# Kernel optimization log

Hardware: AMD Instinct MI355X
Metric: run time of the kernel (lower is better)

## Reference

```python
import jax, jax.numpy as jnp
import numpy as np

N = 50000
E = 800000
NFEAT, NHID, NCLASS = 256, 128, 32


def setup_inputs() -> dict:
    key = jax.random.key(0)
    ks = jax.random.split(key, 8)
    x = jax.random.normal(ks[0], (N, NFEAT), dtype=jnp.float32)
    edge_src = jax.random.randint(ks[1], (E,), 0, N, dtype=jnp.int32)
    edge_dst = jax.random.randint(ks[2], (E,), 0, N, dtype=jnp.int32)
    edge_weight = jax.random.uniform(ks[3], (E,), dtype=jnp.float32)
    # Linear layer params (torch Linear: y = x @ W.T + b); store as [in, out]
    s1 = 1.0 / np.sqrt(NFEAT)
    s2 = 1.0 / np.sqrt(NHID)
    W1 = jax.random.uniform(ks[4], (NFEAT, NHID), jnp.float32, -s1, s1)
    b1 = jax.random.uniform(ks[5], (NHID,), jnp.float32, -s1, s1)
    W2 = jax.random.uniform(ks[6], (NHID, NCLASS), jnp.float32, -s2, s2)
    b2 = jax.random.uniform(ks[7], (NCLASS,), jnp.float32, -s2, s2)
    return {"x": x, "edge_src": edge_src, "edge_dst": edge_dst,
            "edge_weight": edge_weight, "W1": W1, "b1": b1, "W2": W2, "b2": b2}


def spmm(edge_src, edge_dst, edge_weight, h):
    # out[dst] += w * h[src]  -- sparse adjacency @ dense features
    msgs = edge_weight[:, None] * h[edge_src]          # [E, F]
    return jax.ops.segment_sum(msgs, edge_dst, num_segments=N)


def reference(x, edge_src, edge_dst, edge_weight, W1, b1, W2, b2):
    # GCN layer 1: Linear -> SpMM -> ReLU (dropout inactive in eval mode)
    h = x @ W1 + b1                                    # [N, NHID]
    h = spmm(edge_src, edge_dst, edge_weight, h)
    h = jax.nn.relu(h)
    # GCN layer 2: Linear -> SpMM
    h = h @ W2 + b2                                    # [N, NCLASS]
    out = spmm(edge_src, edge_dst, edge_weight, h)
    return out
```

## Files before the change

### kernel.cpp

```cpp
#include <hip/hip_runtime.h>

#define NFEAT 256
#define NHID 128
#define NCLASS 32

typedef __attribute__((ext_vector_type(8))) short short8;
typedef __attribute__((ext_vector_type(4))) float f32x4;
typedef __attribute__((ext_vector_type(4))) int int4v;

static __device__ __forceinline__ unsigned short f2bf(float f) {
    unsigned u = __float_as_uint(f);
    unsigned r = (u + 0x7fffu + ((u >> 16) & 1u)) >> 16;
    return (unsigned short)r;
}
static __device__ __forceinline__ float bf_lo(unsigned d) {
    return __uint_as_float(d << 16);
}
static __device__ __forceinline__ float bf_hi(unsigned d) {
    return __uint_as_float(d & 0xffff0000u);
}

__global__ __launch_bounds__(256) void prep_kernel(
    const float* __restrict__ W1, unsigned short* __restrict__ W1t,
    const int* __restrict__ dst, int* __restrict__ bkt_partial,
    int E, int CE, int shift)
{
    const int tid = threadIdx.x;
    if (blockIdx.x < 128) {
        int o = blockIdx.x * 256 + tid;
        int c = o >> 8, k = o & 255;
        W1t[o] = f2bf(W1[(size_t)k * NHID + c]);
    } else {
        __shared__ int h[256];
        const int kb = blockIdx.x - 128;
        const int start = kb * CE;
        const int end = min(start + CE, E);
        h[tid] = 0;
        __syncthreads();
        for (int e4 = start + tid * 4; e4 < end; e4 += 1024) {
            if (e4 + 3 < end) {
                int4 d4 = *(const int4*)&dst[e4];
                atomicAdd(&h[d4.x >> shift], 1);
                atomicAdd(&h[d4.y >> shift], 1);
                atomicAdd(&h[d4.z >> shift], 1);
                atomicAdd(&h[d4.w >> shift], 1);
            } else {
                for (int e = e4; e < end; ++e)
                    atomicAdd(&h[dst[e] >> shift], 1);
            }
        }
        __syncthreads();
        bkt_partial[kb * 256 + tid] = h[tid];
    }
}

__global__ __launch_bounds__(256) void scan_kernel(
    const int* __restrict__ bkt_partial, int* __restrict__ chunk_pre,
    int* __restrict__ bkt_base, int E)
{
    __shared__ int s[256];
    const int t = threadIdx.x;
    int run = 0;
    for (int kb = 0; kb < 256; ++kb) {
        chunk_pre[kb * 256 + t] = run;
        run += bkt_partial[kb * 256 + t];
    }
    s[t] = run;
    __syncthreads();
    for (int off = 1; off < 256; off <<= 1) {
        int tv = (t >= off) ? s[t - off] : 0;
        __syncthreads();
        s[t] += tv;
        __syncthreads();
    }
    bkt_base[t] = s[t] - run;
    if (t == 255) bkt_base[256] = s[255];
}

__global__ __launch_bounds__(256) void bucket_scatter_kernel(
    const int* __restrict__ src, const int* __restrict__ dst,
    const float* __restrict__ w, const int* __restrict__ bkt_base,
    const int* __restrict__ chunk_pre, uint2* __restrict__ bkt_edges,
    int E, int CE, int shift)
{
    __shared__ int cur[256];
    const int tid = threadIdx.x;
    const int kb = blockIdx.x;
    cur[tid] = bkt_base[tid] + chunk_pre[kb * 256 + tid];
    __syncthreads();
    const int start = kb * CE;
    const int end = min(start + CE, E);
    const unsigned lmask = (1u << shift) - 1u;
    for (int e4 = start + tid * 4; e4 < end; e4 += 1024) {
        if (e4 + 3 < end) {
            int4 d4 = *(const int4*)&dst[e4];
            int4 s4 = *(const int4*)&src[e4];
            float4 w4 = *(const float4*)&w[e4];
            int dd[4] = {d4.x, d4.y, d4.z, d4.w};
            int ss[4] = {s4.x, s4.y, s4.z, s4.w};
            float ww[4] = {w4.x, w4.y, w4.z, w4.w};
#pragma unroll
            for (int j = 0; j < 4; ++j) {
                int b = dd[j] >> shift;
                int pos = atomicAdd(&cur[b], 1);
                uint2 rec;
                rec.x = (unsigned)ss[j] | (((unsigned)dd[j] & lmask) << 24);
                rec.y = __float_as_uint(ww[j]);
                bkt_edges[pos] = rec;
            }
        } else {
            for (int e = e4; e < end; ++e) {
                int d = dst[e];
                int b = d >> shift;
                int pos = atomicAdd(&cur[b], 1);
                uint2 rec;
                rec.x = (unsigned)src[e] | (((unsigned)d & lmask) << 24);
                rec.y = __float_as_uint(w[e]);
                bkt_edges[pos] = rec;
            }
        }
    }
}

__global__ __launch_bounds__(1024) void fine_scatter_kernel(
    const int* __restrict__ bkt_base, const uint2* __restrict__ bkt_edges,
    int* __restrict__ row_ptr, uint2* __restrict__ csr_e,
    int shift, int N, int E)
{
    __shared__ int h[256];
    __shared__ int cur[256];
    const int b = blockIdx.x;
    const int t = threadIdx.x;
    const int lo = bkt_base[b], hi = bkt_base[b + 1];
    const int dbase = b << shift;

    if (t < 256) h[t] = 0;
    __syncthreads();
    for (int i = lo + t; i < hi; i += 1024)
        atomicAdd(&h[bkt_edges[i].x >> 24], 1);
    __syncthreads();
    int v = (t < 256) ? h[t] : 0;
    for (int off = 1; off < 256; off <<= 1) {
        int tv = (t >= off && t < 256) ? h[t - off] : 0;
        __syncthreads();
        if (t < 256) h[t] += tv;
        __syncthreads();
    }
    if (t < 256) {
        int excl = h[t] - v;
        int r = dbase + t;
        if (r < N) row_ptr[r] = lo + excl;
        cur[t] = lo + excl;
    }
    if (b == 0 && t == 0) row_ptr[N] = E;
    __syncthreads();
    for (int i = lo + t; i < hi; i += 1024) {
        uint2 rec = bkt_edges[i];
        int dl = rec.x >> 24;
        int pos = atomicAdd(&cur[dl], 1);
        uint2 o;
        o.x = rec.x & 0xFFFFFFu;
        o.y = rec.y;
        csr_e[pos] = o;
    }
}

__global__ __launch_bounds__(256) void gemm1_mfma_kernel(
    const float* __restrict__ x, const unsigned short* __restrict__ W1t,
    const float* __restrict__ b1, unsigned short* __restrict__ h1b, int N)
{
    __shared__ unsigned short wt[128 * 64];
    __shared__ unsigned short xs[64 * 64];

    const int tid = threadIdx.x;
    const int lane = tid & 63;
    const int wv = tid >> 6;
    const int row0 = blockIdx.x * 64;
    const int l15 = lane & 15;
    const int l47 = lane >> 4;
    const int r7 = lane & 7;

    auto stage_wt = [&](int t) {
#pragma unroll
        for (int j = 0; j < 4; ++j) {
            int si = tid + j * 256;
            int c = si >> 3, s = si & 7;
            int sp = s ^ (c & 7);
            const int4v* wsrc = (const int4v*)(W1t + (size_t)c * 256 + t * 64);
            int4v v = wsrc[s];
            *(int4v*)&wt[c * 64 + sp * 8] = v;
        }
    };
    auto stage_x = [&](int t) {
#pragma unroll
        for (int j = 0; j < 2; ++j) {
            int si = tid + j * 256;
            int r = si >> 3, s = si & 7;
            int row = row0 + r;
            float4 v0 = make_float4(0.f, 0.f, 0.f, 0.f), v1 = v0;
            if (row < N) {
                const float4* xp = (const float4*)&x[(size_t)row * NFEAT + t * 64 + s * 8];
                v0 = xp[0]; v1 = xp[1];
            }
            int w0 = f2bf(v0.x) | ((unsigned)f2bf(v0.y) << 16);
            int w1 = f2bf(v0.z) | ((unsigned)f2bf(v0.w) << 16);
            int w2 = f2bf(v1.x) | ((unsigned)f2bf(v1.y) << 16);
            int w3 = f2bf(v1.z) | ((unsigned)f2bf(v1.w) << 16);
            int sp = s ^ (r & 7);
            int4v pv; pv[0] = w0; pv[1] = w1; pv[2] = w2; pv[3] = w3;
            *(int4v*)&xs[r * 64 + sp * 8] = pv;
        }
    };

    f32x4 acc[8];
#pragma unroll
    for (int cf = 0; cf < 8; ++cf)
#pragma unroll
        for (int r = 0; r < 4; ++r) acc[cf][r] = 0.f;

    const int arow = wv * 16 + l15;
#pragma unroll
    for (int t = 0; t < 4; ++t) {
        stage_wt(t);
        stage_x(t);
        __syncthreads();
        short8 af[2];
#pragma unroll
        for (int kf = 0; kf < 2; ++kf) {
            int slot = (kf * 4 + l47) ^ r7;
            af[kf] = *(const short8*)&xs[arow * 64 + slot * 8];
        }
#pragma unroll
        for (int cf = 0; cf < 8; ++cf) {
            const int brow = cf * 16 + l15;
#pragma unroll
            for (int kf = 0; kf < 2; ++kf) {
                int slot = (kf * 4 + l47) ^ r7;
                short8 bfr = *(const short8*)&wt[brow * 64 + slot * 8];
                acc[cf] = __builtin_amdgcn_mfma_f32_16x16x32_bf16(af[kf], bfr, acc[cf], 0, 0, 0);
            }
        }
        __syncthreads();
    }

#pragma unroll
    for (int cf = 0; cf < 8; ++cf) {
        float bias = b1[cf * 16 + l15];
#pragma unroll
        for (int r = 0; r < 4; ++r) {
            int row = row0 + wv * 16 + l47 * 4 + r;
            if (row < N)
                h1b[(size_t)row * NHID + cf * 16 + l15] = f2bf(acc[cf][r] + bias);
        }
    }
}

__global__ __launch_bounds__(512) void spmm1_gemm2_kernel(
    const int* __restrict__ row_ptr, const uint2* __restrict__ csr_e,
    const unsigned short* __restrict__ h1b, const float* __restrict__ W2,
    const float* __restrict__ b2, unsigned* __restrict__ h2b, int N)
{
    __shared__ float w2s[NHID * NCLASS];
    __shared__ float hrow[8][NHID];
    const int tid = threadIdx.x;
#pragma unroll
    for (int j = 0; j < 8; ++j) {
        int idx = tid + j * 512;
        w2s[idx] = W2[idx];
    }
    __syncthreads();

    const int lane = tid & 63;
    const int wv = tid >> 6;
    const int row = __builtin_amdgcn_readfirstlane(blockIdx.x * 8 + wv);
    if (row >= N) return;

    const int e0 = row_ptr[row], e1 = row_ptr[row + 1];
    const size_t loff = (size_t)(lane * 2);
    float a0 = 0.f, a1 = 0.f;
    int e = e0;
    for (; e + 8 <= e1; e += 8) {
        uint2 r[8];
#pragma unroll
        for (int j = 0; j < 8; ++j) r[j] = csr_e[e + j];
        unsigned d[8];
#pragma unroll
        for (int j = 0; j < 8; ++j)
            d[j] = *(const unsigned*)(h1b + (size_t)r[j].x * NHID + loff);
#pragma unroll
        for (int j = 0; j < 8; ++j) {
            float w = __uint_as_float(r[j].y);
            a0 += w * bf_lo(d[j]); a1 += w * bf_hi(d[j]);
        }
    }
    if (e + 4 <= e1) {
        uint2 r[4];
#pragma unroll
        for (int j = 0; j < 4; ++j) r[j] = csr_e[e + j];
        unsigned d[4];
#pragma unroll
        for (int j = 0; j < 4; ++j)
            d[j] = *(const unsigned*)(h1b + (size_t)r[j].x * NHID + loff);
#pragma unroll
        for (int j = 0; j < 4; ++j) {
            float w = __uint_as_float(r[j].y);
            a0 += w * bf_lo(d[j]); a1 += w * bf_hi(d[j]);
        }
        e += 4;
    }
    if (e + 2 <= e1) {
        uint2 r0 = csr_e[e], r1 = csr_e[e + 1];
        unsigned d0 = *(const unsigned*)(h1b + (size_t)r0.x * NHID + loff);
        unsigned d1 = *(const unsigned*)(h1b + (size_t)r1.x * NHID + loff);
        float w0 = __uint_as_float(r0.y), w1 = __uint_as_float(r1.y);
        a0 += w0 * bf_lo(d0); a1 += w0 * bf_hi(d0);
        a0 += w1 * bf_lo(d1); a1 += w1 * bf_hi(d1);
        e += 2;
    }
    if (e < e1) {
        uint2 r = csr_e[e];
        float w = __uint_as_float(r.y);
        unsigned d = *(const unsigned*)(h1b + (size_t)r.x * NHID + loff);
        a0 += w * bf_lo(d); a1 += w * bf_hi(d);
    }
    *(float2*)&hrow[wv][lane * 2] = make_float2(fmaxf(a0, 0.f), fmaxf(a1, 0.f));

    const int c = lane & 31;
    const int kh = lane >> 5;
    const float* hw = &hrow[wv][kh * 64];
    const float* wp = &w2s[(size_t)kh * 64 * NCLASS + c];
    float acc = 0.f;
#pragma unroll
    for (int k = 0; k < 64; ++k)
        acc += hw[k] * wp[k * NCLASS];
    acc += __shfl(acc, lane ^ 32);
    float accb = acc + b2[c];
    float nb = __shfl(accb, lane ^ 1);
    if (kh == 0 && (lane & 1) == 0) {
        unsigned u = (unsigned)f2bf(accb) | ((unsigned)f2bf(nb) << 16);
        h2b[(size_t)row * 16 + (lane >> 1)] = u;
    }
}

__global__ __launch_bounds__(256) void spmm2_kernel(
    const int* __restrict__ row_ptr, const uint2* __restrict__ csr_e,
    const unsigned* __restrict__ h2b, float* __restrict__ out, int N)
{
    const int li = threadIdx.x & 15;
    const int g = threadIdx.x >> 4;
    const int row = blockIdx.x * 16 + g;
    if (row >= N) return;
    const int e0 = row_ptr[row], e1 = row_ptr[row + 1];
    float a0 = 0.f, a1 = 0.f;
    int e = e0;
    for (; e + 16 <= e1; e += 16) {
        uint2 r[16];
#pragma unroll
        for (int j = 0; j < 16; ++j) r[j] = csr_e[e + j];
        unsigned d[16];
#pragma unroll
        for (int j = 0; j < 16; ++j) d[j] = h2b[(size_t)r[j].x * 16 + li];
#pragma unroll
        for (int j = 0; j < 16; ++j) {
            float w = __uint_as_float(r[j].y);
            a0 += w * bf_lo(d[j]); a1 += w * bf_hi(d[j]);
        }
    }
    for (; e + 8 <= e1; e += 8) {
        uint2 r[8];
#pragma unroll
        for (int j = 0; j < 8; ++j) r[j] = csr_e[e + j];
        unsigned d[8];
#pragma unroll
        for (int j = 0; j < 8; ++j) d[j] = h2b[(size_t)r[j].x * 16 + li];
#pragma unroll
        for (int j = 0; j < 8; ++j) {
            float w = __uint_as_float(r[j].y);
            a0 += w * bf_lo(d[j]); a1 += w * bf_hi(d[j]);
        }
    }
    for (; e + 2 <= e1; e += 2) {
        uint2 r0 = csr_e[e], r1 = csr_e[e + 1];
        unsigned d0 = h2b[(size_t)r0.x * 16 + li];
        unsigned d1 = h2b[(size_t)r1.x * 16 + li];
        float w0 = __uint_as_float(r0.y), w1 = __uint_as_float(r1.y);
        a0 += w0 * bf_lo(d0); a1 += w0 * bf_hi(d0);
        a0 += w1 * bf_lo(d1); a1 += w1 * bf_hi(d1);
    }
    if (e < e1) {
        uint2 r = csr_e[e];
        float w = __uint_as_float(r.y);
        unsigned d = h2b[(size_t)r.x * 16 + li];
        a0 += w * bf_lo(d); a1 += w * bf_hi(d);
    }
    *(float2*)&out[(size_t)row * NCLASS + li * 2] = make_float2(a0, a1);
}


extern "C" void kernel_launch(void* const* d_in, const int* in_sizes, int n_in,
                              void* d_out, int out_size, void* d_ws, size_t ws_size,
                              hipStream_t stream) {
    const float* x    = (const float*)d_in[0];
    const int*   esrc = (const int*)d_in[1];
    const int*   edst = (const int*)d_in[2];
    const float* ew   = (const float*)d_in[3];
    const float* W1   = (const float*)d_in[4];
    const float* b1   = (const float*)d_in[5];
    const float* W2   = (const float*)d_in[6];
    const float* b2   = (const float*)d_in[7];
    float* out = (float*)d_out;

    const int N = in_sizes[0] / NFEAT;
    const int E = in_sizes[1];

    int shift = 0;
    while (((N - 1) >> shift) >= 256) ++shift;
    const int NBKT = ((N - 1) >> shift) + 1;
    const int CE = (((E + 255) / 256) + 3) & ~3;

    char* base = (char*)d_ws;
    size_t off = 0;
    auto take = [&](size_t bytes) -> void* {
        void* p = base + off;
        off += (bytes + 255) & ~(size_t)255;
        return p;
    };
    unsigned short* h1b = (unsigned short*)take((size_t)N * NHID * sizeof(unsigned short));
    unsigned* h2b  = (unsigned*)take((size_t)N * 16 * sizeof(unsigned));
    int*   row_ptr = (int*)take((size_t)(N + 1) * sizeof(int));
    int*   bkt_partial = (int*)take(256 * 256 * sizeof(int));
    int*   chunk_pre   = (int*)take(256 * 256 * sizeof(int));
    int*   bkt_base    = (int*)take(257 * sizeof(int));
    uint2* bkt_edges   = (uint2*)take((size_t)E * sizeof(uint2));
    uint2* csr_e       = (uint2*)take((size_t)E * sizeof(uint2));
    unsigned short* W1t = (unsigned short*)take((size_t)NFEAT * NHID * sizeof(unsigned short));
    (void)ws_size; (void)n_in; (void)out_size;

    prep_kernel<<<384, 256, 0, stream>>>(W1, W1t, edst, bkt_partial, E, CE, shift);
    scan_kernel<<<1, 256, 0, stream>>>(bkt_partial, chunk_pre, bkt_base, E);
    bucket_scatter_kernel<<<256, 256, 0, stream>>>(esrc, edst, ew, bkt_base, chunk_pre,
                                                   bkt_edges, E, CE, shift);
    fine_scatter_kernel<<<NBKT, 1024, 0, stream>>>(bkt_base, bkt_edges, row_ptr, csr_e,
                                                   shift, N, E);
    gemm1_mfma_kernel<<<(N + 63) / 64, 256, 0, stream>>>(x, W1t, b1, h1b, N);
    spmm1_gemm2_kernel<<<(N + 7) / 8, 512, 0, stream>>>(row_ptr, csr_e, h1b, W2, b2, h2b, N);
    spmm2_kernel<<<(N + 15) / 16, 256, 0, stream>>>(row_ptr, csr_e, h2b, out, N);
}
```

Before: 102.7 us.

## Merge bucket scatter and GEMM1 into one launch with block-role dispatch

Combines the coarse edge bucket-scatter kernel and the first MFMA GEMM into a single launch. The first 256 blocks do the scatter and the rest compute GEMM tiles, with shared memory unioned between the two roles. The aim is to run the latency-bound atomic scatter alongside the compute-heavy GEMM and save one kernel launch. The cost is that the scatter blocks now reserve the GEMM's larger shared-memory footprint, which may lower their occupancy.

Result: slower. 111.1 us (+8.1%).

```diff
diff --git a/kernel.cpp b/kernel.cpp
--- a/kernel.cpp
+++ b/kernel.cpp
@@ -77,105 +77,62 @@
     if (t == 255) bkt_base[256] = s[255];
 }
 
-__global__ __launch_bounds__(256) void bucket_scatter_kernel(
+__global__ __launch_bounds__(256) void gemm1_scatter_kernel(
+    const float* __restrict__ x, const unsigned short* __restrict__ W1t,
+    const float* __restrict__ b1, unsigned short* __restrict__ h1b, int N,
     const int* __restrict__ src, const int* __restrict__ dst,
     const float* __restrict__ w, const int* __restrict__ bkt_base,
     const int* __restrict__ chunk_pre, uint2* __restrict__ bkt_edges,
     int E, int CE, int shift)
 {
-    __shared__ int cur[256];
+    __shared__ union SM {
+        struct { unsigned short wt[128 * 64]; unsigned short xs[64 * 64]; } g;
+        int cur[256];
+    } sm;
     const int tid = threadIdx.x;
-    const int kb = blockIdx.x;
-    cur[tid] = bkt_base[tid] + chunk_pre[kb * 256 + tid];
-    __syncthreads();
-    const int start = kb * CE;
-    const int end = min(start + CE, E);
-    const unsigned lmask = (1u << shift) - 1u;
-    for (int e4 = start + tid * 4; e4 < end; e4 += 1024) {
-        if (e4 + 3 < end) {
-            int4 d4 = *(const int4*)&dst[e4];
-            int4 s4 = *(const int4*)&src[e4];
-            float4 w4 = *(const float4*)&w[e4];
-            int dd[4] = {d4.x, d4.y, d4.z, d4.w};
-            int ss[4] = {s4.x, s4.y, s4.z, s4.w};
-            float ww[4] = {w4.x, w4.y, w4.z, w4.w};
-#pragma unroll
-            for (int j = 0; j < 4; ++j) {
-                int b = dd[j] >> shift;
-                int pos = atomicAdd(&cur[b], 1);
-                uint2 rec;
-                rec.x = (unsigned)ss[j] | (((unsigned)dd[j] & lmask) << 24);
-                rec.y = __float_as_uint(ww[j]);
-                bkt_edges[pos] = rec;
+
+    if (blockIdx.x < 256) {
+        const int kb = blockIdx.x;
+        sm.cur[tid] = bkt_base[tid] + chunk_pre[kb * 256 + tid];
+        __syncthreads();
+        const int start = kb * CE;
+        const int end = min(start + CE, E);
+        const unsigned lmask = (1u << shift) - 1u;
+        for (int e4 = start + tid * 4; e4 < end; e4 += 1024) {
+            if (e4 + 3 < end) {
+                int4 d4 = *(const int4*)&dst[e4];
+                int4 s4 = *(const int4*)&src[e4];
+                float4 w4 = *(const float4*)&w[e4];
+                int dd[4] = {d4.x, d4.y, d4.z, d4.w};
+                int ss[4] = {s4.x, s4.y, s4.z, s4.w};
+                float ww[4] = {w4.x, w4.y, w4.z, w4.w};
+#pragma unroll
+                for (int j = 0; j < 4; ++j) {
+                    int b = dd[j] >> shift;
+                    int pos = atomicAdd(&sm.cur[b], 1);
+                    uint2 rec;
+                    rec.x = (unsigned)ss[j] | (((unsigned)dd[j] & lmask) << 24);
+                    rec.y = __float_as_uint(ww[j]);
+                    bkt_edges[pos] = rec;
+                }
+            } else {
+                for (int e = e4; e < end; ++e) {
+                    int d = dst[e];
+                    int b = d >> shift;
+                    int pos = atomicAdd(&sm.cur[b], 1);
+                    uint2 rec;
+                    rec.x = (unsigned)src[e] | (((unsigned)d & lmask) << 24);
+                    rec.y = __float_as_uint(w[e]);
+                    bkt_edges[pos] = rec;
+                }
             }
-        } else {
-            for (int e = e4; e < end; ++e) {
-                int d = dst[e];
-                int b = d >> shift;
-                int pos = atomicAdd(&cur[b], 1);
-                uint2 rec;
-                rec.x = (unsigned)src[e] | (((unsigned)d & lmask) << 24);
-                rec.y = __float_as_uint(w[e]);
-                bkt_edges[pos] = rec;
-            }
-        }
-    }
-}
-
-__global__ __launch_bounds__(1024) void fine_scatter_kernel(
-    const int* __restrict__ bkt_base, const uint2* __restrict__ bkt_edges,
-    int* __restrict__ row_ptr, uint2* __restrict__ csr_e,
-    int shift, int N, int E)
-{
-    __shared__ int h[256];
-    __shared__ int cur[256];
-    const int b = blockIdx.x;
-    const int t = threadIdx.x;
-    const int lo = bkt_base[b], hi = bkt_base[b + 1];
-    const int dbase = b << shift;
-
-    if (t < 256) h[t] = 0;
-    __syncthreads();
-    for (int i = lo + t; i < hi; i += 1024)
-        atomicAdd(&h[bkt_edges[i].x >> 24], 1);
-    __syncthreads();
-    int v = (t < 256) ? h[t] : 0;
-    for (int off = 1; off < 256; off <<= 1) {
-        int tv = (t >= off && t < 256) ? h[t - off] : 0;
-        __syncthreads();
-        if (t < 256) h[t] += tv;
-        __syncthreads();
-    }
-    if (t < 256) {
-        int excl = h[t] - v;
-        int r = dbase + t;
-        if (r < N) row_ptr[r] = lo + excl;
-        cur[t] = lo + excl;
-    }
-    if (b == 0 && t == 0) row_ptr[N] = E;
-    __syncthreads();
-    for (int i = lo + t; i < hi; i += 1024) {
-        uint2 rec = bkt_edges[i];
-        int dl = rec.x >> 24;
-        int pos = atomicAdd(&cur[dl], 1);
-        uint2 o;
-        o.x = rec.x & 0xFFFFFFu;
-        o.y = rec.y;
-        csr_e[pos] = o;
-    }
-}
-
-__global__ __launch_bounds__(256) void gemm1_mfma_kernel(
-    const float* __restrict__ x, const unsigned short* __restrict__ W1t,
-    const float* __restrict__ b1, unsigned short* __restrict__ h1b, int N)
-{
-    __shared__ unsigned short wt[128 * 64];
-    __shared__ unsigned short xs[64 * 64];
-
-    const int tid = threadIdx.x;
+        }
+        return;
+    }
+
     const int lane = tid & 63;
     const int wv = tid >> 6;
-    const int row0 = blockIdx.x * 64;
+    const int row0 = (blockIdx.x - 256) * 64;
     const int l15 = lane & 15;
     const int l47 = lane >> 4;
     const int r7 = lane & 7;
@@ -188,7 +145,7 @@
             int sp = s ^ (c & 7);
             const int4v* wsrc = (const int4v*)(W1t + (size_t)c * 256 + t * 64);
             int4v v = wsrc[s];
-            *(int4v*)&wt[c * 64 + sp * 8] = v;
+            *(int4v*)&sm.g.wt[c * 64 + sp * 8] = v;
         }
     };
     auto stage_x = [&](int t) {
@@ -208,7 +165,7 @@
             int w3 = f2bf(v1.z) | ((unsigned)f2bf(v1.w) << 16);
             int sp = s ^ (r & 7);
             int4v pv; pv[0] = w0; pv[1] = w1; pv[2] = w2; pv[3] = w3;
-            *(int4v*)&xs[r * 64 + sp * 8] = pv;
+            *(int4v*)&sm.g.xs[r * 64 + sp * 8] = pv;
         }
     };
 
@@ -228,7 +185,7 @@
 #pragma unroll
         for (int kf = 0; kf < 2; ++kf) {
             int slot = (kf * 4 + l47) ^ r7;
-            af[kf] = *(const short8*)&xs[arow * 64 + slot * 8];
+            af[kf] = *(const short8*)&sm.g.xs[arow * 64 + slot * 8];
         }
 #pragma unroll
         for (int cf = 0; cf < 8; ++cf) {
@@ -236,7 +193,7 @@
 #pragma unroll
             for (int kf = 0; kf < 2; ++kf) {
                 int slot = (kf * 4 + l47) ^ r7;
-                short8 bfr = *(const short8*)&wt[brow * 64 + slot * 8];
+                short8 bfr = *(const short8*)&sm.g.wt[brow * 64 + slot * 8];
                 acc[cf] = __builtin_amdgcn_mfma_f32_16x16x32_bf16(af[kf], bfr, acc[cf], 0, 0, 0);
             }
         }
@@ -252,6 +209,49 @@
             if (row < N)
                 h1b[(size_t)row * NHID + cf * 16 + l15] = f2bf(acc[cf][r] + bias);
         }
+    }
+}
+
+__global__ __launch_bounds__(1024) void fine_scatter_kernel(
+    const int* __restrict__ bkt_base, const uint2* __restrict__ bkt_edges,
+    int* __restrict__ row_ptr, uint2* __restrict__ csr_e,
+    int shift, int N, int E)
+{
+    __shared__ int h[256];
+    __shared__ int cur[256];
+    const int b = blockIdx.x;
+    const int t = threadIdx.x;
+    const int lo = bkt_base[b], hi = bkt_base[b + 1];
+    const int dbase = b << shift;
+
+    if (t < 256) h[t] = 0;
+    __syncthreads();
+    for (int i = lo + t; i < hi; i += 1024)
+        atomicAdd(&h[bkt_edges[i].x >> 24], 1);
+    __syncthreads();
+    int v = (t < 256) ? h[t] : 0;
+    for (int off = 1; off < 256; off <<= 1) {
+        int tv = (t >= off && t < 256) ? h[t - off] : 0;
+        __syncthreads();
+        if (t < 256) h[t] += tv;
+        __syncthreads();
+    }
+    if (t < 256) {
+        int excl = h[t] - v;
+        int r = dbase + t;
+        if (r < N) row_ptr[r] = lo + excl;
+        cur[t] = lo + excl;
+    }
+    if (b == 0 && t == 0) row_ptr[N] = E;
+    __syncthreads();
+    for (int i = lo + t; i < hi; i += 1024) {
+        uint2 rec = bkt_edges[i];
+        int dl = rec.x >> 24;
+        int pos = atomicAdd(&cur[dl], 1);
+        uint2 o;
+        o.x = rec.x & 0xFFFFFFu;
+        o.y = rec.y;
+        csr_e[pos] = o;
     }
 }
 
@@ -417,6 +417,7 @@
     while (((N - 1) >> shift) >= 256) ++shift;
     const int NBKT = ((N - 1) >> shift) + 1;
     const int CE = (((E + 255) / 256) + 3) & ~3;
+    const int ntiles = (N + 63) / 64;
 
     char* base = (char*)d_ws;
     size_t off = 0;
@@ -438,11 +439,10 @@
 
     prep_kernel<<<384, 256, 0, stream>>>(W1, W1t, edst, bkt_partial, E, CE, shift);
     scan_kernel<<<1, 256, 0, stream>>>(bkt_partial, chunk_pre, bkt_base, E);
-    bucket_scatter_kernel<<<256, 256, 0, stream>>>(esrc, edst, ew, bkt_base, chunk_pre,
-                                                   bkt_edges, E, CE, shift);
+    gemm1_scatter_kernel<<<256 + ntiles, 256, 0, stream>>>(
+        x, W1t, b1, h1b, N, esrc, edst, ew, bkt_base, chunk_pre, bkt_edges, E, CE, shift);
     fine_scatter_kernel<<<NBKT, 1024, 0, stream>>>(bkt_base, bkt_edges, row_ptr, csr_e,
                                                    shift, N, E);
-    gemm1_mfma_kernel<<<(N + 63) / 64, 256, 0, stream>>>(x, W1t, b1, h1b, N);
     spmm1_gemm2_kernel<<<(N + 7) / 8, 512, 0, stream>>>(row_ptr, csr_e, h1b, W2, b2, h2b, N);
     spmm2_kernel<<<(N + 15) / 16, 256, 0, stream>>>(row_ptr, csr_e, h2b, out, N);
 }
```
